# Kernel optimization log

Measured on AMD Instinct MI355X. Metric: run time of the kernel, lower is better.

The kernel has to match this reference:

```python
import jax, jax.numpy as jnp
import numpy as np

N_NODE = 4096
K = 32           # num_nearest_neighbors
HIDDEN = 128
RMS_EPS = 1e-5
DT = 0.01        # init scale for linear weights (init_linear_weights(..., scale=dt))


def _rmsnorm(x, g):
    # RMSNorm over last dim with learned scale (eqx.nn.RMSNorm-style)
    return x * jax.lax.rsqrt(jnp.mean(x * x, axis=-1, keepdims=True) + RMS_EPS) * g


def _pos_mlp(x, W1, b1, g1, W2, b2, g2, W3, b3):
    # MLPWithLayerNorm(in=2, width=HIDDEN, depth=2, out=1, act=silu, rms_norm=True):
    # per hidden layer: Linear -> RMSNorm -> SiLU; final Linear with identity activation.
    h = jax.nn.silu(_rmsnorm(x @ W1.T + b1, g1))
    h = jax.nn.silu(_rmsnorm(h @ W2.T + b2, g2))
    return h @ W3.T + b3  # [E, 1]


def setup_inputs() -> dict:
    key = jax.random.key(0)
    ks = jax.random.split(key, 8)

    def xavier(k, shape):
        fan_in, fan_out = shape[1], shape[0]
        std = jnp.sqrt(2.0 / (fan_in + fan_out))
        return (jax.random.normal(k, shape, dtype=jnp.float32) * std * DT)

    return {
        "pos": jax.random.normal(ks[0], (N_NODE, 3), dtype=jnp.float32),
        "t": jax.random.uniform(ks[1], (1,), dtype=jnp.float32),
        "W1": xavier(ks[2], (HIDDEN, 2)),
        "b1": jnp.zeros((HIDDEN,), dtype=jnp.float32),
        "g1": jnp.ones((HIDDEN,), dtype=jnp.float32),
        "W2": xavier(ks[3], (HIDDEN, HIDDEN)),
        "b2": jnp.zeros((HIDDEN,), dtype=jnp.float32),
        "g2": jnp.ones((HIDDEN,), dtype=jnp.float32),
        "W3": xavier(ks[4], (1, HIDDEN)),
        "b3": jnp.zeros((1,), dtype=jnp.float32),
    }


def reference(pos, t, W1, b1, g1, W2, b2, g2, W3, b3):
    n = pos.shape[0]
    # Pairwise squared distances for kNN graph build
    diff = pos[:, None, :] - pos[None, :, :]              # [n, n, 3]
    radial_full = jnp.sum(diff * diff, axis=-1)           # [n, n]
    masked = radial_full.at[jnp.diag_indices(n)].set(jnp.inf)
    _, recv = jax.lax.top_k(-masked, k=K)                 # [n, K] nearest neighbors
    senders = jnp.repeat(jnp.arange(n), K)                # [n*K]
    receivers = recv.reshape(-1)                          # [n*K]

    # Gather edge geometry (normalize=False)
    coord_diff = pos[senders] - pos[receivers]            # [E, 3]
    radial = jnp.sum(coord_diff * coord_diff, axis=1, keepdims=True)  # [E, 1]

    # Per-edge MLP on [radial, t]
    t_scalar = jnp.reshape(t, ())
    edge_features = jnp.concatenate(
        [radial, jnp.full_like(radial, t_scalar)], axis=-1)          # [E, 2]
    edge_scalars = _pos_mlp(edge_features, W1, b1, g1, W2, b2, g2, W3, b3).squeeze(-1)

    # Scatter-sum messages back to sender nodes, average by neighbor count
    trans = coord_diff * edge_scalars[:, None]            # [E, 3]
    seg_sum = jax.ops.segment_sum(trans, senders, num_segments=n)    # [n, 3]
    seg_count = jnp.maximum(float(K), 1.0)
    return pos + seg_sum / seg_count
```

## Files before the change

kernel.cpp:

```cpp
#include <hip/hip_runtime.h>
#include <stdint.h>

#define NN   4096
#define KK   32
#define HID  128
#define BLK  256
#define WPB  4
#define GRID (NN / WPB)
#define CAP  128

typedef unsigned short bf16_t;
typedef __attribute__((ext_vector_type(8))) short bf16x8;
typedef __attribute__((ext_vector_type(4))) float f32x4;
typedef __attribute__((ext_vector_type(2))) float f32x2;

#define FINF __uint_as_float(0x7f800000u)

__device__ __forceinline__ uint32_t pk2bf(float lo, float hi) {
    uint32_t r;
    asm("v_cvt_pk_bf16_f32 %0, %1, %2" : "=v"(r) : "v"(lo), "v"(hi));
    return r;
}
__device__ __forceinline__ float fastrcp(float x) {
    float r; asm("v_rcp_f32 %0, %1" : "=v"(r) : "v"(x)); return r;
}
__device__ __forceinline__ float fastrsq(float x) {
    float r; asm("v_rsq_f32 %0, %1" : "=v"(r) : "v"(x)); return r;
}
__device__ __forceinline__ float siluf(float x) {
    return x * fastrcp(1.0f + __expf(-x));
}
__device__ __forceinline__ f32x2 pk_add(f32x2 a, f32x2 b) {
    f32x2 r; asm("v_pk_add_f32 %0, %1, %2" : "=v"(r) : "v"(a), "v"(b)); return r;
}
__device__ __forceinline__ f32x2 pk_sq(f32x2 a) {
    f32x2 r; asm("v_pk_mul_f32 %0, %1, %1" : "=v"(r) : "v"(a)); return r;
}

template<int CTRL>
__device__ __forceinline__ float rsum_step(float x) {
    return x + __int_as_float(__builtin_amdgcn_update_dpp(
        0, __float_as_int(x), CTRL, 0xF, 0xF, true));
}
__device__ __forceinline__ float rowsum16(float x) {
    x = rsum_step<0xB1>(x);
    x = rsum_step<0x4E>(x);
    x = rsum_step<0x124>(x);
    x = rsum_step<0x128>(x);
    return x;
}
__device__ __forceinline__ float wsum64(float x) {
    x = rowsum16(x);
    x += __shfl_xor(x, 16, 64);
    x += __shfl_xor(x, 32, 64);
    return x;
}

__device__ __forceinline__ void dist4s(const float4* __restrict__ p4, int g, int lane,
                                       float px, float py, float pz, float d[4]) {
    float4 f0 = p4[g*192 + 3*lane];
    float4 f1 = p4[g*192 + 3*lane + 1];
    float4 f2 = p4[g*192 + 3*lane + 2];
    float jx[4] = {f0.x, f0.w, f1.z, f2.y};
    float jy[4] = {f0.y, f1.x, f1.w, f2.z};
    float jz[4] = {f0.z, f1.y, f2.x, f2.w};
    #pragma unroll
    for (int c = 0; c < 4; ++c) {
        float dx = px - jx[c], dy = py - jy[c], dz = pz - jz[c];
        d[c] = __fadd_rn(__fadd_rn(__fmul_rn(dx,dx), __fmul_rn(dy,dy)),
                         __fmul_rn(dz,dz));
    }
}

__global__ __launch_bounds__(256) void prepack_w2(
    const float* __restrict__ W2, uint4* __restrict__ w2b)
{
    int c  = blockIdx.x * 256 + threadIdx.x;
    int f  = c >> 6, ln = c & 63;
    int NT = f >> 2, kk = f & 3;
    int row = NT*16 + (ln & 15);
    int k0  = kk*32 + (ln >> 4) * 8;
    const float* s = W2 + row * HID + k0;
    float4 lo = *(const float4*)s;
    float4 hi = *(const float4*)(s + 4);
    uint4 pk;
    pk.x = pk2bf(lo.x, lo.y);
    pk.y = pk2bf(lo.z, lo.w);
    pk.z = pk2bf(hi.x, hi.y);
    pk.w = pk2bf(hi.z, hi.w);
    w2b[c] = pk;
}

template<bool WS>
struct __align__(16) Sm {
    union __align__(16) U {
        ushort dbf[NN];
        ushort h1[KK * HID];
    } uw[WPB];
    uint32_t cand[WPB][CAP];
    uint32_t ccnt[WPB];
    float    rads[WPB][KK];
    float    sedge[WPB][KK];
    int      recvs[WPB][KK];
    uint32_t w2l[WS ? 4 : HID * 64];
};

template<bool WS>
__global__ __launch_bounds__(BLK) void egnn_main(
    const float* __restrict__ pos, const float* __restrict__ tptr,
    const float* __restrict__ W1,  const float* __restrict__ b1,
    const float* __restrict__ g1,  const float* __restrict__ W2,
    const float* __restrict__ b2,  const float* __restrict__ g2,
    const float* __restrict__ W3,  const float* __restrict__ b3,
    const uint4* __restrict__ w2b, float* __restrict__ out)
{
    __shared__ Sm<WS> sm;
    const int tid  = threadIdx.x;
    const int lane = tid & 63;
    const int wid  = tid >> 6;
    const int i    = blockIdx.x * WPB + wid;
    const int l15  = lane & 15, lq = lane >> 4;

    {
        const int ph = ((blockIdx.x & 3) + (blockIdx.x >> 8)) & 3;
        for (int k = 0; k < ph; ++k) __builtin_amdgcn_s_sleep(11);
    }

    if (lane == 0) sm.ccnt[wid] = 0;

    const float ts  = tptr[0];
    const float b3s = b3[0];

    float A2, AC, C2;
    {
        const float4 w1v = ((const float4*)W1)[lane];
        const float2 b1v = ((const float2*)b1)[lane];
        float t0 = ts * w1v.y + b1v.x;
        float t1 = ts * w1v.w + b1v.y;
        A2 = wsum64(w1v.x*w1v.x + w1v.z*w1v.z);
        AC = wsum64(w1v.x*t0    + w1v.z*t1);
        C2 = wsum64(t0*t0       + t1*t1);
    }

    if constexpr (!WS) {
        for (int idx = tid; idx < HID * 16; idx += BLK) {
            int row = idx >> 4, c = idx & 15;
            const float* src = W2 + row * HID + c * 8;
            float4 lo = *(const float4*)src;
            float4 hi = *(const float4*)(src + 4);
            uint4 pk;
            pk.x = pk2bf(lo.x, lo.y);
            pk.y = pk2bf(lo.z, lo.w);
            pk.z = pk2bf(hi.x, hi.y);
            pk.w = pk2bf(hi.z, hi.w);
            *((uint4*)&sm.w2l[row * 64 + 4 * (c ^ (row & 15))]) = pk;
        }
        __syncthreads();
    }

    const float px = pos[3*i], py = pos[3*i+1], pz = pos[3*i+2];
    const float4* p4 = (const float4*)pos;
    const f32x2 nPxy = {-px, -py}, nPzx = {-pz, -px}, nPyz = {-py, -pz};

    const int  sgrp     = i >> 8;
    const bool selfLane = ((i >> 2) & 63) == lane;
    const int  selfc    = i & 3;

    float mind = FINF;
    {
        ushort* dbf = sm.uw[wid].dbf;
        #pragma unroll 4
        for (int g = 0; g < 16; ++g) {
            float4 f0 = p4[g*192 + 3*lane];
            float4 f1 = p4[g*192 + 3*lane+1];
            float4 f2 = p4[g*192 + 3*lane+2];
            f32x2 S0 = pk_sq(pk_add(f32x2{f0.x, f0.y}, nPxy));
            f32x2 S1 = pk_sq(pk_add(f32x2{f0.z, f0.w}, nPzx));
            f32x2 S2 = pk_sq(pk_add(f32x2{f1.x, f1.y}, nPyz));
            f32x2 S3 = pk_sq(pk_add(f32x2{f1.z, f1.w}, nPxy));
            f32x2 S4 = pk_sq(pk_add(f32x2{f2.x, f2.y}, nPzx));
            f32x2 S5 = pk_sq(pk_add(f32x2{f2.z, f2.w}, nPyz));
            float d0 = S0.x + S0.y + S1.x;
            float d1 = S1.y + S2.x + S2.y;
            float d2 = S3.x + S3.y + S4.x;
            float d3 = S4.y + S5.x + S5.y;
            if (g == sgrp && selfLane) {
                d0 = (selfc == 0) ? FINF : d0;
                d1 = (selfc == 1) ? FINF : d1;
                d2 = (selfc == 2) ? FINF : d2;
                d3 = (selfc == 3) ? FINF : d3;
            }
            uint32_t lo = __builtin_amdgcn_perm(__float_as_uint(d1),
                                                __float_as_uint(d0), 0x07060302u);
            uint32_t hi = __builtin_amdgcn_perm(__float_as_uint(d3),
                                                __float_as_uint(d2), 0x07060302u);
            *((uint2*)&dbf[g*256 + 4*lane]) = make_uint2(lo, hi);
            mind = fminf(fminf(fminf(mind, d0), fminf(d1, d2)), d3);
        }
    }
    const uint32_t m16 = __float_as_uint(mind) >> 16;

    uint32_t v = 0;
    #pragma unroll
    for (int b = 15; b >= 0; --b) {
        uint32_t t = v | (1u << b);
        int nl = (int)__popcll(__ballot(m16 < t));
        if (nl < KK) v = t;
    }

    uint32_t cnt;
    {
        const ushort* dbf = sm.uw[wid].dbf;
        const uint32_t vk  = (v << 16) | 0xffffu;
        const uint32_t jb0 = 4*lane;
        #pragma unroll 4
        for (int g = 0; g < 16; ++g) {
            uint2 w = *((const uint2*)&dbf[g*256 + 4*lane]);
            uint32_t jb = jb0 + g*256;
            uint32_t k0 = (w.x << 16) | jb;
            uint32_t k1 = (w.x & 0xffff0000u) | (jb + 1);
            uint32_t k2 = (w.y << 16) | (jb + 2);
            uint32_t k3 = (w.y & 0xffff0000u) | (jb + 3);
            if (k0 <= vk) { uint32_t s = atomicAdd(&sm.ccnt[wid], 1u);
                            if (s < CAP) sm.cand[wid][s] = k0; }
            if (k1 <= vk) { uint32_t s = atomicAdd(&sm.ccnt[wid], 1u);
                            if (s < CAP) sm.cand[wid][s] = k1; }
            if (k2 <= vk) { uint32_t s = atomicAdd(&sm.ccnt[wid], 1u);
                            if (s < CAP) sm.cand[wid][s] = k2; }
            if (k3 <= vk) { uint32_t s = atomicAdd(&sm.ccnt[wid], 1u);
                            if (s < CAP) sm.cand[wid][s] = k3; }
        }
        cnt = sm.ccnt[wid];
    }
    const int cntv = (int)cnt;

    if (cntv <= CAP) {
        for (int idx = cntv + lane; idx < CAP; idx += 64)
            sm.cand[wid][idx] = 0xffffffffu;

        const int nb = (cntv + 15) >> 4;
        #pragma unroll
        for (int h = 0; h < 2; ++h) {
            int idx = h*64 + lane;
            if (idx < cntv) {
                uint32_t km = sm.cand[wid][idx];
                int rank = 0;
                for (int q = 0; q < nb; ++q) {
                    const uint4* cp = (const uint4*)&sm.cand[wid][q*16];
                    uint4 u0 = cp[0];
                    uint4 u1 = cp[1];
                    uint4 u2 = cp[2];
                    uint4 u3 = cp[3];
                    rank += (u0.x < km) ? 1 : 0;
                    rank += (u0.y < km) ? 1 : 0;
                    rank += (u0.z < km) ? 1 : 0;
                    rank += (u0.w < km) ? 1 : 0;
                    rank += (u1.x < km) ? 1 : 0;
                    rank += (u1.y < km) ? 1 : 0;
                    rank += (u1.z < km) ? 1 : 0;
                    rank += (u1.w < km) ? 1 : 0;
                    rank += (u2.x < km) ? 1 : 0;
                    rank += (u2.y < km) ? 1 : 0;
                    rank += (u2.z < km) ? 1 : 0;
                    rank += (u2.w < km) ? 1 : 0;
                    rank += (u3.x < km) ? 1 : 0;
                    rank += (u3.y < km) ? 1 : 0;
                    rank += (u3.z < km) ? 1 : 0;
                    rank += (u3.w < km) ? 1 : 0;
                }
                if (rank < KK) sm.recvs[wid][rank] = (int)(km & 0xFFFFu);
            }
        }
    } else {
        unsigned long long locmask = 0ull;
        if (selfLane)
            locmask |= 1ull << ((sgrp << 2) | selfc);
        for (int it = 0; it < KK; ++it) {
            unsigned long long best = ~0ull;
            for (int g = 0; g < 16; ++g) {
                float d[4];
                dist4s(p4, g, lane, px, py, pz, d);
                #pragma unroll
                for (int c = 0; c < 4; ++c) {
                    bool dead = ((locmask >> (g*4 + c)) & 1ull) != 0ull;
                    unsigned long long key = dead ? ~0ull
                        : ((((unsigned long long)__float_as_uint(d[c])) << 12)
                           | (unsigned)(g*256 + 4*lane + c));
                    best = best < key ? best : key;
                }
            }
            #pragma unroll
            for (int m = 32; m >= 1; m >>= 1) {
                unsigned long long o = __shfl_xor(best, m, 64);
                best = best < o ? best : o;
            }
            int j = (int)(best & 0xfffull);
            if (lane == 0) sm.recvs[wid][it] = j;
            if (((j >> 2) & 63) == lane)
                locmask |= 1ull << ((j >> 8) * 4 + (j & 3));
        }
    }

    float cdx = 0.f, cdy = 0.f, cdz = 0.f;
    if (lane < KK) {
        int r = sm.recvs[wid][lane];
        cdx = px - pos[3*r];
        cdy = py - pos[3*r+1];
        cdz = pz - pos[3*r+2];
        float rad = __fadd_rn(__fadd_rn(__fmul_rn(cdx,cdx), __fmul_rn(cdy,cdy)),
                              __fmul_rn(cdz,cdz));
        sm.rads[wid][lane] = rad;
    }

    {
        const int ch = lane >> 2, epr = lane & 3;
        float4 wA = ((const float4*)W1)[ch*4    ];
        float4 wB = ((const float4*)W1)[ch*4 + 1];
        float4 wC = ((const float4*)W1)[ch*4 + 2];
        float4 wD = ((const float4*)W1)[ch*4 + 3];
        float4 bA = ((const float4*)b1)[ch*2], bB = ((const float4*)b1)[ch*2 + 1];
        float4 gA = ((const float4*)g1)[ch*2], gB = ((const float4*)g1)[ch*2 + 1];
        float av[8] = {wA.x, wA.z, wB.x, wB.z, wC.x, wC.z, wD.x, wD.z};
        float cv[8] = {ts*wA.y + bA.x, ts*wA.w + bA.y, ts*wB.y + bA.z, ts*wB.w + bA.w,
                       ts*wC.y + bB.x, ts*wC.w + bB.y, ts*wD.y + bB.z, ts*wD.w + bB.w};
        float gv[8] = {gA.x, gA.y, gA.z, gA.w, gB.x, gB.y, gB.z, gB.w};
        uint4* h1q = (uint4*)&sm.uw[wid].h1[0];
        #pragma unroll
        for (int g = 0; g < 8; ++g) {
            int E = 4*g + epr;
            float rad = sm.rads[wid][E];
            float sqv = rad*rad*A2 + 2.0f*rad*AC + C2;
            float rn  = fastrsq(sqv * (1.0f/HID) + 1e-5f);
            uint32_t pk[4];
            #pragma unroll
            for (int p = 0; p < 4; ++p) {
                float va = siluf((rad*av[2*p]   + cv[2*p])   * rn * gv[2*p]);
                float vb = siluf((rad*av[2*p+1] + cv[2*p+1]) * rn * gv[2*p+1]);
                pk[p] = pk2bf(va, vb);
            }
            h1q[E*16 + (ch ^ (E & 15))] = uint4{pk[0], pk[1], pk[2], pk[3]};
        }
    }

    float g2v[8], w3v[8], b2v[8];
    #pragma unroll
    for (int nt = 0; nt < 8; ++nt) {
        int n = nt*16 + l15;
        g2v[nt] = g2[n]; w3v[nt] = W3[n]; b2v[nt] = b2[n];
    }

    const bf16x8* h1v = (const bf16x8*)&sm.uw[wid].h1[0];
    #pragma unroll
    for (int mt = 0; mt < 2; ++mt) {
        f32x4 acc[8];
        #pragma unroll
        for (int nt = 0; nt < 8; ++nt) acc[nt] = f32x4{0.f, 0.f, 0.f, 0.f};
        const int m = mt*16 + l15;
        if constexpr (WS) {
            const bf16x8* bv = (const bf16x8*)w2b;
            #pragma unroll
            for (int kk = 0; kk < 4; ++kk) {
                bf16x8 af = h1v[m*16 + ((kk*4 + lq) ^ l15)];
                #pragma unroll
                for (int nt = 0; nt < 8; ++nt)
                    acc[nt] = __builtin_amdgcn_mfma_f32_16x16x32_bf16(
                                  af, bv[(nt*4 + kk)*64 + lane], acc[nt], 0, 0, 0);
            }
        } else {
            const bf16x8* w2v = (const bf16x8*)sm.w2l;
            #pragma unroll
            for (int kk = 0; kk < 4; ++kk) {
                const int q = (kk*4 + lq) ^ l15;
                bf16x8 af = h1v[m*16 + q];
                #pragma unroll
                for (int nt = 0; nt < 8; ++nt)
                    acc[nt] = __builtin_amdgcn_mfma_f32_16x16x32_bf16(
                                  af, w2v[(nt*16 + l15)*16 + q], acc[nt], 0, 0, 0);
            }
        }

        float ss[4];
        #pragma unroll
        for (int r = 0; r < 4; ++r) {
            float t = 0.f;
            #pragma unroll
            for (int nt = 0; nt < 8; ++nt) {
                float zz = acc[nt][r] + b2v[nt];
                acc[nt][r] = zz;
                t += zz*zz;
            }
            ss[r] = rowsum16(t);
        }
        float sp[4];
        #pragma unroll
        for (int r = 0; r < 4; ++r) {
            float rn = fastrsq(ss[r] * (1.0f/HID) + 1e-5f);
            float t = 0.f;
            #pragma unroll
            for (int nt = 0; nt < 8; ++nt)
                t += siluf(acc[nt][r] * rn * g2v[nt]) * w3v[nt];
            sp[r] = rowsum16(t);
        }
        if (l15 == 0) {
            #pragma unroll
            for (int r = 0; r < 4; ++r)
                sm.sedge[wid][mt*16 + lq*4 + r] = sp[r] + b3s;
        }
    }

    float mx = 0.f, my = 0.f, mz = 0.f;
    if (lane < KK) {
        float s = sm.sedge[wid][lane];
        mx = cdx * s; my = cdy * s; mz = cdz * s;
    }
    mx = wsum64(mx);
    my = wsum64(my);
    mz = wsum64(mz);
    if (lane == 0) {
        out[3*i    ] = px + mx * (1.0f/KK);
        out[3*i + 1] = py + my * (1.0f/KK);
        out[3*i + 2] = pz + mz * (1.0f/KK);
    }
}

extern "C" void kernel_launch(void* const* d_in, const int* in_sizes, int n_in,
                              void* d_out, int out_size, void* d_ws, size_t ws_size,
                              hipStream_t stream) {
    (void)in_sizes; (void)n_in; (void)out_size;
    const float* pos = (const float*)d_in[0];
    const float* t   = (const float*)d_in[1];
    const float* W1  = (const float*)d_in[2];
    const float* b1  = (const float*)d_in[3];
    const float* g1  = (const float*)d_in[4];
    const float* W2  = (const float*)d_in[5];
    const float* b2  = (const float*)d_in[6];
    const float* g2  = (const float*)d_in[7];
    const float* W3  = (const float*)d_in[8];
    const float* b3  = (const float*)d_in[9];
    float* out = (float*)d_out;

    if (d_ws != nullptr && ws_size >= 32768) {
        prepack_w2<<<8, 256, 0, stream>>>(W2, (uint4*)d_ws);
        egnn_main<true><<<GRID, BLK, 0, stream>>>(
            pos, t, W1, b1, g1, W2, b2, g2, W3, b3, (const uint4*)d_ws, out);
    } else {
        egnn_main<false><<<GRID, BLK, 0, stream>>>(
            pos, t, W1, b1, g1, W2, b2, g2, W3, b3, nullptr, out);
    }
}
```

Baseline: 105.6 us.

## Split each node across two wavefronts and keep distances in registers

Each node is now handled by two wavefronts instead of one. Each wave computes half of the 4096 distances and keeps the packed bf16 keys in registers rather than staging them in LDS. The per-lane minima, candidate list, ranking, MLP M-tiles and final reduction are shared through LDS with block-wide barriers. The goal is to halve the serial per-node latency and cut LDS use so occupancy rises. In exchange it adds several __syncthreads, doubles the grid size, and drops the staggered-start sleep.

Result: faster. 99.30 us (-6.0%).

```diff
diff --git a/kernel.cpp b/kernel.cpp
--- a/kernel.cpp
+++ b/kernel.cpp
@@ -5,8 +5,8 @@
 #define KK   32
 #define HID  128
 #define BLK  256
-#define WPB  4
-#define GRID (NN / WPB)
+#define NPB  2
+#define GRID (NN / NPB)
 #define CAP  128
 
 typedef unsigned short bf16_t;
@@ -93,15 +93,14 @@
 
 template<bool WS>
 struct __align__(16) Sm {
-    union __align__(16) U {
-        ushort dbf[NN];
-        ushort h1[KK * HID];
-    } uw[WPB];
-    uint32_t cand[WPB][CAP];
-    uint32_t ccnt[WPB];
-    float    rads[WPB][KK];
-    float    sedge[WPB][KK];
-    int      recvs[WPB][KK];
+    ushort   h1[NPB][KK * HID];
+    uint32_t cand[NPB][CAP];
+    uint32_t ccnt[NPB];
+    ushort   smin[NPB][2][64];
+    float    rads[NPB][KK];
+    float    sedge[NPB][KK];
+    int      recvs[NPB][KK];
+    float    partial[NPB][2][4];
     uint32_t w2l[WS ? 4 : HID * 64];
 };
 
@@ -118,15 +117,12 @@
     const int tid  = threadIdx.x;
     const int lane = tid & 63;
     const int wid  = tid >> 6;
-    const int i    = blockIdx.x * WPB + wid;
+    const int p    = wid >> 1;
+    const int sub  = wid & 1;
+    const int i    = blockIdx.x * NPB + p;
     const int l15  = lane & 15, lq = lane >> 4;
 
-    {
-        const int ph = ((blockIdx.x & 3) + (blockIdx.x >> 8)) & 3;
-        for (int k = 0; k < ph; ++k) __builtin_amdgcn_s_sleep(11);
-    }
-
-    if (lane == 0) sm.ccnt[wid] = 0;
+    if (tid < NPB) sm.ccnt[tid] = 0;
 
     const float ts  = tptr[0];
     const float b3s = b3[0];
@@ -155,7 +151,6 @@
             pk.w = pk2bf(hi.z, hi.w);
             *((uint4*)&sm.w2l[row * 64 + 4 * (c ^ (row & 15))]) = pk;
         }
-        __syncthreads();
     }
 
     const float px = pos[3*i], py = pos[3*i+1], pz = pos[3*i+2];
@@ -166,39 +161,44 @@
     const bool selfLane = ((i >> 2) & 63) == lane;
     const int  selfc    = i & 3;
 
+    uint32_t dlo[8], dhi[8];
     float mind = FINF;
+    #pragma unroll
+    for (int gg = 0; gg < 8; ++gg) {
+        const int g = sub*8 + gg;
+        float4 f0 = p4[g*192 + 3*lane];
+        float4 f1 = p4[g*192 + 3*lane+1];
+        float4 f2 = p4[g*192 + 3*lane+2];
+        f32x2 S0 = pk_sq(pk_add(f32x2{f0.x, f0.y}, nPxy));
+        f32x2 S1 = pk_sq(pk_add(f32x2{f0.z, f0.w}, nPzx));
+        f32x2 S2 = pk_sq(pk_add(f32x2{f1.x, f1.y}, nPyz));
+        f32x2 S3 = pk_sq(pk_add(f32x2{f1.z, f1.w}, nPxy));
+        f32x2 S4 = pk_sq(pk_add(f32x2{f2.x, f2.y}, nPzx));
+        f32x2 S5 = pk_sq(pk_add(f32x2{f2.z, f2.w}, nPyz));
+        float d0 = S0.x + S0.y + S1.x;
+        float d1 = S1.y + S2.x + S2.y;
+        float d2 = S3.x + S3.y + S4.x;
+        float d3 = S4.y + S5.x + S5.y;
+        if (g == sgrp && selfLane) {
+            d0 = (selfc == 0) ? FINF : d0;
+            d1 = (selfc == 1) ? FINF : d1;
+            d2 = (selfc == 2) ? FINF : d2;
+            d3 = (selfc == 3) ? FINF : d3;
+        }
+        dlo[gg] = __builtin_amdgcn_perm(__float_as_uint(d1),
+                                        __float_as_uint(d0), 0x07060302u);
+        dhi[gg] = __builtin_amdgcn_perm(__float_as_uint(d3),
+                                        __float_as_uint(d2), 0x07060302u);
+        mind = fminf(fminf(fminf(mind, d0), fminf(d1, d2)), d3);
+    }
+    const uint32_t m16own = __float_as_uint(mind) >> 16;
+    sm.smin[p][sub][lane] = (ushort)m16own;
+    __syncthreads();
+    uint32_t m16;
     {
-        ushort* dbf = sm.uw[wid].dbf;
-        #pragma unroll 4
-        for (int g = 0; g < 16; ++g) {
-            float4 f0 = p4[g*192 + 3*lane];
-            float4 f1 = p4[g*192 + 3*lane+1];
-            float4 f2 = p4[g*192 + 3*lane+2];
-            f32x2 S0 = pk_sq(pk_add(f32x2{f0.x, f0.y}, nPxy));
-            f32x2 S1 = pk_sq(pk_add(f32x2{f0.z, f0.w}, nPzx));
-            f32x2 S2 = pk_sq(pk_add(f32x2{f1.x, f1.y}, nPyz));
-            f32x2 S3 = pk_sq(pk_add(f32x2{f1.z, f1.w}, nPxy));
-            f32x2 S4 = pk_sq(pk_add(f32x2{f2.x, f2.y}, nPzx));
-            f32x2 S5 = pk_sq(pk_add(f32x2{f2.z, f2.w}, nPyz));
-            float d0 = S0.x + S0.y + S1.x;
-            float d1 = S1.y + S2.x + S2.y;
-            float d2 = S3.x + S3.y + S4.x;
-            float d3 = S4.y + S5.x + S5.y;
-            if (g == sgrp && selfLane) {
-                d0 = (selfc == 0) ? FINF : d0;
-                d1 = (selfc == 1) ? FINF : d1;
-                d2 = (selfc == 2) ? FINF : d2;
-                d3 = (selfc == 3) ? FINF : d3;
-            }
-            uint32_t lo = __builtin_amdgcn_perm(__float_as_uint(d1),
-                                                __float_as_uint(d0), 0x07060302u);
-            uint32_t hi = __builtin_amdgcn_perm(__float_as_uint(d3),
-                                                __float_as_uint(d2), 0x07060302u);
-            *((uint2*)&dbf[g*256 + 4*lane]) = make_uint2(lo, hi);
-            mind = fminf(fminf(fminf(mind, d0), fminf(d1, d2)), d3);
-        }
-    }
-    const uint32_t m16 = __float_as_uint(mind) >> 16;
+        uint32_t o = (uint32_t)sm.smin[p][sub ^ 1][lane];
+        m16 = m16own < o ? m16own : o;
+    }
 
     uint32_t v = 0;
     #pragma unroll
@@ -208,70 +208,63 @@
         if (nl < KK) v = t;
     }
 
-    uint32_t cnt;
     {
-        const ushort* dbf = sm.uw[wid].dbf;
-        const uint32_t vk  = (v << 16) | 0xffffu;
-        const uint32_t jb0 = 4*lane;
-        #pragma unroll 4
-        for (int g = 0; g < 16; ++g) {
-            uint2 w = *((const uint2*)&dbf[g*256 + 4*lane]);
-            uint32_t jb = jb0 + g*256;
-            uint32_t k0 = (w.x << 16) | jb;
-            uint32_t k1 = (w.x & 0xffff0000u) | (jb + 1);
-            uint32_t k2 = (w.y << 16) | (jb + 2);
-            uint32_t k3 = (w.y & 0xffff0000u) | (jb + 3);
-            if (k0 <= vk) { uint32_t s = atomicAdd(&sm.ccnt[wid], 1u);
-                            if (s < CAP) sm.cand[wid][s] = k0; }
-            if (k1 <= vk) { uint32_t s = atomicAdd(&sm.ccnt[wid], 1u);
-                            if (s < CAP) sm.cand[wid][s] = k1; }
-            if (k2 <= vk) { uint32_t s = atomicAdd(&sm.ccnt[wid], 1u);
-                            if (s < CAP) sm.cand[wid][s] = k2; }
-            if (k3 <= vk) { uint32_t s = atomicAdd(&sm.ccnt[wid], 1u);
-                            if (s < CAP) sm.cand[wid][s] = k3; }
-        }
-        cnt = sm.ccnt[wid];
-    }
-    const int cntv = (int)cnt;
+        const uint32_t vk = (v << 16) | 0xffffu;
+        #pragma unroll
+        for (int gg = 0; gg < 8; ++gg) {
+            uint32_t jb = (uint32_t)((sub*8 + gg)*256 + 4*lane);
+            uint32_t k0 = (dlo[gg] << 16) | jb;
+            uint32_t k1 = (dlo[gg] & 0xffff0000u) | (jb + 1);
+            uint32_t k2 = (dhi[gg] << 16) | (jb + 2);
+            uint32_t k3 = (dhi[gg] & 0xffff0000u) | (jb + 3);
+            if (k0 <= vk) { uint32_t s = atomicAdd(&sm.ccnt[p], 1u);
+                            if (s < CAP) sm.cand[p][s] = k0; }
+            if (k1 <= vk) { uint32_t s = atomicAdd(&sm.ccnt[p], 1u);
+                            if (s < CAP) sm.cand[p][s] = k1; }
+            if (k2 <= vk) { uint32_t s = atomicAdd(&sm.ccnt[p], 1u);
+                            if (s < CAP) sm.cand[p][s] = k2; }
+            if (k3 <= vk) { uint32_t s = atomicAdd(&sm.ccnt[p], 1u);
+                            if (s < CAP) sm.cand[p][s] = k3; }
+        }
+    }
+    __syncthreads();
+    const int cntv = (int)sm.ccnt[p];
 
     if (cntv <= CAP) {
         for (int idx = cntv + lane; idx < CAP; idx += 64)
-            sm.cand[wid][idx] = 0xffffffffu;
+            sm.cand[p][idx] = 0xffffffffu;
 
         const int nb = (cntv + 15) >> 4;
-        #pragma unroll
-        for (int h = 0; h < 2; ++h) {
-            int idx = h*64 + lane;
-            if (idx < cntv) {
-                uint32_t km = sm.cand[wid][idx];
-                int rank = 0;
-                for (int q = 0; q < nb; ++q) {
-                    const uint4* cp = (const uint4*)&sm.cand[wid][q*16];
-                    uint4 u0 = cp[0];
-                    uint4 u1 = cp[1];
-                    uint4 u2 = cp[2];
-                    uint4 u3 = cp[3];
-                    rank += (u0.x < km) ? 1 : 0;
-                    rank += (u0.y < km) ? 1 : 0;
-                    rank += (u0.z < km) ? 1 : 0;
-                    rank += (u0.w < km) ? 1 : 0;
-                    rank += (u1.x < km) ? 1 : 0;
-                    rank += (u1.y < km) ? 1 : 0;
-                    rank += (u1.z < km) ? 1 : 0;
-                    rank += (u1.w < km) ? 1 : 0;
-                    rank += (u2.x < km) ? 1 : 0;
-                    rank += (u2.y < km) ? 1 : 0;
-                    rank += (u2.z < km) ? 1 : 0;
-                    rank += (u2.w < km) ? 1 : 0;
-                    rank += (u3.x < km) ? 1 : 0;
-                    rank += (u3.y < km) ? 1 : 0;
-                    rank += (u3.z < km) ? 1 : 0;
-                    rank += (u3.w < km) ? 1 : 0;
-                }
-                if (rank < KK) sm.recvs[wid][rank] = (int)(km & 0xFFFFu);
-            }
-        }
-    } else {
+        const int idx = sub*64 + lane;
+        if (idx < cntv) {
+            uint32_t km = sm.cand[p][idx];
+            int rank = 0;
+            for (int q = 0; q < nb; ++q) {
+                const uint4* cp = (const uint4*)&sm.cand[p][q*16];
+                uint4 u0 = cp[0];
+                uint4 u1 = cp[1];
+                uint4 u2 = cp[2];
+                uint4 u3 = cp[3];
+                rank += (u0.x < km) ? 1 : 0;
+                rank += (u0.y < km) ? 1 : 0;
+                rank += (u0.z < km) ? 1 : 0;
+                rank += (u0.w < km) ? 1 : 0;
+                rank += (u1.x < km) ? 1 : 0;
+                rank += (u1.y < km) ? 1 : 0;
+                rank += (u1.z < km) ? 1 : 0;
+                rank += (u1.w < km) ? 1 : 0;
+                rank += (u2.x < km) ? 1 : 0;
+                rank += (u2.y < km) ? 1 : 0;
+                rank += (u2.z < km) ? 1 : 0;
+                rank += (u2.w < km) ? 1 : 0;
+                rank += (u3.x < km) ? 1 : 0;
+                rank += (u3.y < km) ? 1 : 0;
+                rank += (u3.z < km) ? 1 : 0;
+                rank += (u3.w < km) ? 1 : 0;
+            }
+            if (rank < KK) sm.recvs[p][rank] = (int)(km & 0xFFFFu);
+        }
+    } else if (sub == 0) {
         unsigned long long locmask = 0ull;
         if (selfLane)
             locmask |= 1ull << ((sgrp << 2) | selfc);
@@ -295,21 +288,23 @@
                 best = best < o ? best : o;
             }
             int j = (int)(best & 0xfffull);
-            if (lane == 0) sm.recvs[wid][it] = j;
+            if (lane == 0) sm.recvs[p][it] = j;
             if (((j >> 2) & 63) == lane)
                 locmask |= 1ull << ((j >> 8) * 4 + (j & 3));
         }
     }
+    __syncthreads();
 
     float cdx = 0.f, cdy = 0.f, cdz = 0.f;
-    if (lane < KK) {
-        int r = sm.recvs[wid][lane];
+    if (lane < 16) {
+        int e = sub*16 + lane;
+        int r = sm.recvs[p][e];
         cdx = px - pos[3*r];
         cdy = py - pos[3*r+1];
         cdz = pz - pos[3*r+2];
         float rad = __fadd_rn(__fadd_rn(__fmul_rn(cdx,cdx), __fmul_rn(cdy,cdy)),
                               __fmul_rn(cdz,cdz));
-        sm.rads[wid][lane] = rad;
+        sm.rads[p][e] = rad;
     }
 
     {
@@ -324,19 +319,19 @@
         float cv[8] = {ts*wA.y + bA.x, ts*wA.w + bA.y, ts*wB.y + bA.z, ts*wB.w + bA.w,
                        ts*wC.y + bB.x, ts*wC.w + bB.y, ts*wD.y + bB.z, ts*wD.w + bB.w};
         float gv[8] = {gA.x, gA.y, gA.z, gA.w, gB.x, gB.y, gB.z, gB.w};
-        uint4* h1q = (uint4*)&sm.uw[wid].h1[0];
+        uint4* h1q = (uint4*)&sm.h1[p][0];
         #pragma unroll
-        for (int g = 0; g < 8; ++g) {
-            int E = 4*g + epr;
-            float rad = sm.rads[wid][E];
+        for (int g2i = 0; g2i < 4; ++g2i) {
+            int E = sub*16 + 4*g2i + epr;
+            float rad = sm.rads[p][E];
             float sqv = rad*rad*A2 + 2.0f*rad*AC + C2;
             float rn  = fastrsq(sqv * (1.0f/HID) + 1e-5f);
             uint32_t pk[4];
             #pragma unroll
-            for (int p = 0; p < 4; ++p) {
-                float va = siluf((rad*av[2*p]   + cv[2*p])   * rn * gv[2*p]);
-                float vb = siluf((rad*av[2*p+1] + cv[2*p+1]) * rn * gv[2*p+1]);
-                pk[p] = pk2bf(va, vb);
+            for (int pp = 0; pp < 4; ++pp) {
+                float va = siluf((rad*av[2*pp]   + cv[2*pp])   * rn * gv[2*pp]);
+                float vb = siluf((rad*av[2*pp+1] + cv[2*pp+1]) * rn * gv[2*pp+1]);
+                pk[pp] = pk2bf(va, vb);
             }
             h1q[E*16 + (ch ^ (E & 15))] = uint4{pk[0], pk[1], pk[2], pk[3]};
         }
@@ -349,13 +344,12 @@
         g2v[nt] = g2[n]; w3v[nt] = W3[n]; b2v[nt] = b2[n];
     }
 
-    const bf16x8* h1v = (const bf16x8*)&sm.uw[wid].h1[0];
-    #pragma unroll
-    for (int mt = 0; mt < 2; ++mt) {
+    const bf16x8* h1v = (const bf16x8*)&sm.h1[p][0];
+    {
         f32x4 acc[8];
         #pragma unroll
         for (int nt = 0; nt < 8; ++nt) acc[nt] = f32x4{0.f, 0.f, 0.f, 0.f};
-        const int m = mt*16 + l15;
+        const int m = sub*16 + l15;
         if constexpr (WS) {
             const bf16x8* bv = (const bf16x8*)w2b;
             #pragma unroll
@@ -404,22 +398,31 @@
         if (l15 == 0) {
             #pragma unroll
             for (int r = 0; r < 4; ++r)
-                sm.sedge[wid][mt*16 + lq*4 + r] = sp[r] + b3s;
+                sm.sedge[p][sub*16 + lq*4 + r] = sp[r] + b3s;
         }
     }
 
     float mx = 0.f, my = 0.f, mz = 0.f;
-    if (lane < KK) {
-        float s = sm.sedge[wid][lane];
+    if (lane < 16) {
+        float s = sm.sedge[p][sub*16 + lane];
         mx = cdx * s; my = cdy * s; mz = cdz * s;
     }
     mx = wsum64(mx);
     my = wsum64(my);
     mz = wsum64(mz);
     if (lane == 0) {
-        out[3*i    ] = px + mx * (1.0f/KK);
-        out[3*i + 1] = py + my * (1.0f/KK);
-        out[3*i + 2] = pz + mz * (1.0f/KK);
+        sm.partial[p][sub][0] = mx;
+        sm.partial[p][sub][1] = my;
+        sm.partial[p][sub][2] = mz;
+    }
+    __syncthreads();
+    if (sub == 0 && lane == 0) {
+        float fx = sm.partial[p][0][0] + sm.partial[p][1][0];
+        float fy = sm.partial[p][0][1] + sm.partial[p][1][1];
+        float fz = sm.partial[p][0][2] + sm.partial[p][1][2];
+        out[3*i    ] = px + fx * (1.0f/KK);
+        out[3*i + 1] = py + fy * (1.0f/KK);
+        out[3*i + 2] = pz + fz * (1.0f/KK);
     }
 }
 
```
